# Kernel optimization log

Hardware: AMD Instinct MI355X
Metric: run time of the kernel (lower is better)

Reference implementation:

```python
import jax, jax.numpy as jnp
import numpy as np

BATCH, N_IN, N_OUT = 1024, 512, 512
GRID, DEGREE = 8, 3
NUM_BASIS = GRID + DEGREE  # 11
LO, HI = -3.0, 3.0
_h = (HI - LO) / GRID
# extended knot vector: GRID + 2*DEGREE + 1 knots -> GRID + DEGREE basis functions
KNOTS = jnp.asarray(np.linspace(LO - DEGREE * _h, HI + DEGREE * _h,
                                GRID + 2 * DEGREE + 1), dtype=jnp.float32)


def bspline_basis(x):
    """Cox-de Boor recursion. x: (batch, n_in) -> (batch, n_in, NUM_BASIS)."""
    t = KNOTS
    xb = x[..., None]
    B = ((xb >= t[:-1]) & (xb < t[1:])).astype(x.dtype)  # degree 0
    for d in range(1, DEGREE + 1):
        left = (xb - t[:-(d + 1)]) / (t[d:-1] - t[:-(d + 1)])
        right = (t[d + 1:] - xb) / (t[d + 1:] - t[1:-d])
        B = left * B[..., :-1] + right * B[..., 1:]
    return B


def setup_inputs() -> dict:
    key = jax.random.key(0)
    kx, kc, kw = jax.random.split(key, 3)
    x = jax.random.normal(kx, (BATCH, N_IN), dtype=jnp.float32)
    # xavier_normal_ init for c: fan_in = num_basis, fan_out = n_in*n_out
    c_std = float(np.sqrt(2.0 / (N_IN * N_OUT + NUM_BASIS)))
    c = jax.random.normal(kc, (N_IN * N_OUT, NUM_BASIS), dtype=jnp.float32) * c_std
    w_std = float(np.sqrt(2.0 / (N_IN + N_OUT)))
    w = jax.random.normal(kw, (N_IN, N_OUT), dtype=jnp.float32) * w_std
    return {"x": x, "c": c, "w": w}


def reference(x, c, w):
    # spline basis: (batch, n_in, K)
    bx = bspline_basis(x)
    # per-edge coefficients: (n_in, n_out, K)
    cr = c.reshape(N_IN, N_OUT, NUM_BASIS)
    # out[b,i,o] = sum_k bx[b,i,k] * c[i,o,k]
    spline = jnp.einsum('bik,iok->bio', bx, cr)
    # w * (silu(x) + spline), summed over n_in -> (batch, n_out)
    out = jnp.einsum('io,bio->bo', w, jax.nn.silu(x)[..., None] + spline)
    return out
```

## Files before the change

### kernel.cpp

```cpp
#include <hip/hip_runtime.h>

#define BATCH 1024
#define NIN   512
#define NOUT  512
#define NB    11
#define KDIM  (NIN * 12)
#define SPLITS 16
#define IPS    (NIN / SPLITS)
#define LDW    104

typedef short bf16x8 __attribute__((ext_vector_type(8)));
typedef float f32x4  __attribute__((ext_vector_type(4)));
typedef unsigned short ushort8 __attribute__((ext_vector_type(8)));

__device__ __forceinline__ unsigned short f2bf(float f) {
  unsigned u = __float_as_uint(f);
  u += 0x7fff + ((u >> 16) & 1);
  return (unsigned short)(u >> 16);
}
__device__ __forceinline__ float bf2f(unsigned short h) {
  return __uint_as_float((unsigned)h << 16);
}

__global__ __launch_bounds__(256) void k_prep(const float* __restrict__ c,
                                              const float* __restrict__ w,
                                              unsigned short* __restrict__ Bt) {
  __shared__ float          ws_[8 * 128];
  __shared__ unsigned short sbt[128 * 96];
  int tid = threadIdx.x;
  int bc  = blockIdx.x;
  int i0  = (bc >> 2) * 8;
  int o0  = (bc & 3) * 128;
  {
    int r = tid >> 5, oq = (tid & 31) * 4;
    *(f32x4*)&ws_[r * 128 + oq] = *(const f32x4*)&w[(size_t)(i0 + r) * NOUT + o0 + oq];
  }
  __syncthreads();
  for (int n = 0; n < 11; ++n) {
    int ch  = n * 256 + tid;
    int il  = ch / 352;
    int off = (ch - il * 352) * 4;
    f32x4 cv = *(const f32x4*)&c[(size_t)(i0 + il) * (NIN * NB) + (size_t)o0 * NB + off];
#pragma unroll
    for (int e = 0; e < 4; ++e) {
      int t  = off + e;
      int op = t / 11;
      int k  = t - op * 11;
      sbt[op * 96 + il * 12 + k] = f2bf(cv[e] * ws_[il * 128 + op]);
    }
  }
  {
    int il = tid >> 5, oq = (tid & 31) * 4;
#pragma unroll
    for (int e = 0; e < 4; ++e)
      sbt[(oq + e) * 96 + il * 12 + 11] = f2bf(ws_[il * 128 + oq + e]);
  }
  __syncthreads();
  for (int n = 0; n < 6; ++n) {
    int ch = n * 256 + tid;
    int op = ch / 12, q = ch - op * 12;
    *(ushort8*)&Bt[(size_t)(o0 + op) * KDIM + i0 * 12 + q * 8] =
        *(const ushort8*)&sbt[op * 96 + q * 8];
  }
}

__global__ __launch_bounds__(256) void k_fused(const float* __restrict__ x,
                                               const unsigned short* __restrict__ Bt,
                                               unsigned short* __restrict__ part,
                                               float* __restrict__ out,
                                               int splits, int ipersplit) {
  __shared__ unsigned short As[128 * LDW];
  __shared__ unsigned short Bs[128 * LDW];
  const int tid  = threadIdx.x;
  const int lane = tid & 63, wave = tid >> 6;
  const int wr = wave >> 1, wc = wave & 1;
  const int mbase = blockIdx.x * 128, nbase = blockIdx.y * 128;
  const int split = blockIdx.z;
  const int istart = split * ipersplit;

  f32x4 acc[4][4] = {};
  const int mrow = lane & 15;
  const int kq   = (lane >> 4) * 8;

  const int iters = ipersplit / 8;
  for (int it = 0; it < iters; ++it) {
    int ib = istart + it * 8;
    {
      int bl  = tid >> 1;
      int il0 = (tid & 1) * 4;
      f32x4 xv = *(const f32x4*)&x[(size_t)(mbase + bl) * NIN + ib + il0];
      unsigned short* arow = &As[bl * LDW];
#pragma unroll
      for (int q = 0; q < 4; ++q) {
        int col = (il0 + q) * 12;
        *(unsigned long long*)&arow[col]     = 0ULL;
        *(unsigned long long*)&arow[col + 4] = 0ULL;
        *(unsigned long long*)&arow[col + 8] = 0ULL;
        float xq = xv[q];
        float um = (xq + 5.25f) * (1.0f / 0.75f);
        int   m  = (int)floorf(um);
        if (m >= 0 && m <= 13) {
          float u  = um - (float)m;
          float u2 = u * u, u3 = u2 * u;
          float omu = 1.0f - u;
          float w3 = u3 * (1.0f / 6.0f);
          float w2 = (-3.0f*u3 + 3.0f*u2 + 3.0f*u + 1.0f) * (1.0f/6.0f);
          float w1 = (3.0f*u3 - 6.0f*u2 + 4.0f) * (1.0f/6.0f);
          float w0 = omu * omu * omu * (1.0f / 6.0f);
          int j0 = m - 3;
          if (j0 >= 0 && j0 <= 10)         arow[col + j0]     = f2bf(w0);
          if (j0 + 1 >= 0 && j0 + 1 <= 10) arow[col + j0 + 1] = f2bf(w1);
          if (j0 + 2 >= 0 && j0 + 2 <= 10) arow[col + j0 + 2] = f2bf(w2);
          if (m <= 10)                     arow[col + m]      = f2bf(w3);
        }
        float sig = 1.0f / (1.0f + __expf(-xq));
        arow[col + 11] = f2bf(xq * sig);
      }
    }
#pragma unroll
    for (int n = 0; n < 6; ++n) {
      int ch  = n * 256 + tid;
      int row = ch / 12;
      int cg  = ch - row * 12;
      ushort8 vb = *(const ushort8*)&Bt[(size_t)(nbase + row) * KDIM + ib * 12 + cg * 8];
      *(ushort8*)&Bs[row * LDW + cg * 8] = vb;
    }
    __syncthreads();

#pragma unroll
    for (int ks = 0; ks < 96; ks += 32) {
      bf16x8 af[4], bfr[4];
#pragma unroll
      for (int mt = 0; mt < 4; ++mt)
        af[mt] = *(const bf16x8*)&As[(wr * 64 + mt * 16 + mrow) * LDW + ks + kq];
#pragma unroll
      for (int nt = 0; nt < 4; ++nt)
        bfr[nt] = *(const bf16x8*)&Bs[(wc * 64 + nt * 16 + mrow) * LDW + ks + kq];
#pragma unroll
      for (int mt = 0; mt < 4; ++mt)
#pragma unroll
        for (int nt = 0; nt < 4; ++nt)
          acc[mt][nt] = __builtin_amdgcn_mfma_f32_16x16x32_bf16(af[mt], bfr[nt], acc[mt][nt], 0, 0, 0);
    }
    __syncthreads();
  }

  const int rq = (lane >> 4) * 4;
  if (splits == 1) {
#pragma unroll
    for (int mt = 0; mt < 4; ++mt)
#pragma unroll
      for (int nt = 0; nt < 4; ++nt) {
        int colg = nbase + wc * 64 + nt * 16 + mrow;
#pragma unroll
        for (int r = 0; r < 4; ++r) {
          int rowg = mbase + wr * 64 + mt * 16 + rq + r;
          out[(size_t)rowg * NOUT + colg] = acc[mt][nt][r];
        }
      }
    return;
  }
#pragma unroll
  for (int mt = 0; mt < 4; ++mt)
#pragma unroll
    for (int nt = 0; nt < 4; ++nt) {
      int colg = nbase + wc * 64 + nt * 16 + mrow;
#pragma unroll
      for (int r = 0; r < 4; ++r) {
        int rowg = mbase + wr * 64 + mt * 16 + rq + r;
        part[((size_t)split * BATCH + rowg) * NOUT + colg] = f2bf(acc[mt][nt][r]);
      }
    }
}

__global__ __launch_bounds__(256) void k_reduce(const unsigned short* __restrict__ part,
                                                float* __restrict__ out) {
  int t = blockIdx.x * 256 + threadIdx.x;
  const ushort8* pv = (const ushort8*)part;
  float s[8] = {};
#pragma unroll
  for (int sp = 0; sp < SPLITS; ++sp) {
    ushort8 v = pv[(size_t)sp * (BATCH * NOUT / 8) + t];
#pragma unroll
    for (int e = 0; e < 8; ++e) s[e] += bf2f(v[e]);
  }
  f32x4 lo = { s[0], s[1], s[2], s[3] };
  f32x4 hi = { s[4], s[5], s[6], s[7] };
  ((f32x4*)out)[t * 2]     = lo;
  ((f32x4*)out)[t * 2 + 1] = hi;
}

extern "C" void kernel_launch(void* const* d_in, const int* in_sizes, int n_in,
                              void* d_out, int out_size, void* d_ws, size_t ws_size,
                              hipStream_t stream) {
  const float* x = (const float*)d_in[0];
  const float* c = (const float*)d_in[1];
  const float* w = (const float*)d_in[2];
  float* out = (float*)d_out;

  unsigned short* Bt = (unsigned short*)d_ws;
  size_t off_part = (size_t)NOUT * KDIM * 2;
  unsigned short* part = (unsigned short*)((char*)d_ws + off_part);
  size_t need = off_part + (size_t)SPLITS * BATCH * NOUT * 2;

  k_prep<<<dim3(256), 256, 0, stream>>>(c, w, Bt);
  if (ws_size >= need) {
    k_fused<<<dim3(8, 4, SPLITS), 256, 0, stream>>>(x, Bt, part, out, SPLITS, IPS);
    k_reduce<<<dim3((BATCH * NOUT / 8) / 256), 256, 0, stream>>>(part, out);
  } else {
    k_fused<<<dim3(8, 4, 1), 256, 0, stream>>>(x, Bt, part, out, 1, NIN);
  }
}
```

Measured before the change: 92.46 us.

## Fuse prep, GEMM and reduce into one cooperative kernel with grid syncs

Replaces the three separate launches (coefficient prep, split-K GEMM, reduction) with a single cooperative kernel of 512 blocks that runs the three phases separated by grid.sync(). The prep phase is re-tiled to 4 input rows per block so that 512 blocks cover it. The aim is to remove launch gaps and kernel boundaries between the stages. In exchange it depends on cooperative launch succeeding with 512 co-resident blocks, which use about 53KB of LDS each, and adds grid-wide barrier costs. If the cooperative launch fails it falls back to the old path.

```diff
diff --git a/kernel.cpp b/kernel.cpp
--- a/kernel.cpp
+++ b/kernel.cpp
@@ -1,4 +1,7 @@
 #include <hip/hip_runtime.h>
+#include <hip/hip_cooperative_groups.h>
+
+namespace cg = cooperative_groups;
 
 #define BATCH 1024
 #define NIN   512
@@ -21,6 +24,174 @@
 __device__ __forceinline__ float bf2f(unsigned short h) {
   return __uint_as_float((unsigned)h << 16);
 }
+
+
+__device__ __forceinline__ void basis_row_gen(const float* __restrict__ x,
+                                              unsigned short* __restrict__ As,
+                                              int tid, int mbase, int ib) {
+  int bl  = tid >> 1;
+  int il0 = (tid & 1) * 4;
+  f32x4 xv = *(const f32x4*)&x[(size_t)(mbase + bl) * NIN + ib + il0];
+  unsigned short* arow = &As[bl * LDW];
+#pragma unroll
+  for (int q = 0; q < 4; ++q) {
+    int col = (il0 + q) * 12;
+    *(unsigned long long*)&arow[col]     = 0ULL;
+    *(unsigned long long*)&arow[col + 4] = 0ULL;
+    *(unsigned long long*)&arow[col + 8] = 0ULL;
+    float xq = xv[q];
+    float um = (xq + 5.25f) * (1.0f / 0.75f);
+    int   m  = (int)floorf(um);
+    if (m >= 0 && m <= 13) {
+      float u  = um - (float)m;
+      float u2 = u * u, u3 = u2 * u;
+      float omu = 1.0f - u;
+      float w3 = u3 * (1.0f / 6.0f);
+      float w2 = (-3.0f*u3 + 3.0f*u2 + 3.0f*u + 1.0f) * (1.0f/6.0f);
+      float w1 = (3.0f*u3 - 6.0f*u2 + 4.0f) * (1.0f/6.0f);
+      float w0 = omu * omu * omu * (1.0f / 6.0f);
+      int j0 = m - 3;
+      if (j0 >= 0 && j0 <= 10)         arow[col + j0]     = f2bf(w0);
+      if (j0 + 1 >= 0 && j0 + 1 <= 10) arow[col + j0 + 1] = f2bf(w1);
+      if (j0 + 2 >= 0 && j0 + 2 <= 10) arow[col + j0 + 2] = f2bf(w2);
+      if (m <= 10)                     arow[col + m]      = f2bf(w3);
+    }
+    float sig = 1.0f / (1.0f + __expf(-xq));
+    arow[col + 11] = f2bf(xq * sig);
+  }
+}
+
+__global__ __launch_bounds__(256) void k_mega(const float* __restrict__ x,
+                                              const float* __restrict__ c,
+                                              const float* __restrict__ w,
+                                              unsigned short* __restrict__ Bt,
+                                              unsigned short* __restrict__ part,
+                                              float* __restrict__ out) {
+  __shared__ char smem[53248];
+  cg::grid_group grid = cg::this_grid();
+  const int blk = blockIdx.x;
+  const int tid = threadIdx.x;
+
+  {
+    float*          ws_ = (float*)smem;
+    unsigned short* sbt = (unsigned short*)(smem + 2048);
+    int i0 = (blk >> 2) * 4;
+    int o0 = (blk & 3) * 128;
+    if (tid < 128) {
+      int il = tid >> 5, oq = (tid & 31) * 4;
+      *(f32x4*)&ws_[il * 128 + oq] = *(const f32x4*)&w[(size_t)(i0 + il) * NOUT + o0 + oq];
+    }
+    __syncthreads();
+    for (int n = 0; n < 6; ++n) {
+      int ch = n * 256 + tid;
+      if (ch < 1408) {
+        int il  = ch / 352;
+        int off = (ch - il * 352) * 4;
+        f32x4 cv = *(const f32x4*)&c[(size_t)(i0 + il) * (NIN * NB) + (size_t)o0 * NB + off];
+#pragma unroll
+        for (int e = 0; e < 4; ++e) {
+          int t  = off + e;
+          int op = t / 11;
+          int k  = t - op * 11;
+          sbt[op * 48 + il * 12 + k] = f2bf(cv[e] * ws_[il * 128 + op]);
+        }
+      }
+    }
+#pragma unroll
+    for (int e = 0; e < 2; ++e) {
+      int idx = e * 256 + tid;
+      int op = idx >> 2, il = idx & 3;
+      sbt[op * 48 + il * 12 + 11] = f2bf(ws_[il * 128 + op]);
+    }
+    __syncthreads();
+    for (int n = 0; n < 3; ++n) {
+      int ch = n * 256 + tid;
+      int op = ch / 6, q = ch - op * 6;
+      *(ushort8*)&Bt[(size_t)(o0 + op) * KDIM + i0 * 12 + q * 8] =
+          *(const ushort8*)&sbt[op * 48 + q * 8];
+    }
+  }
+  grid.sync();
+
+  {
+    unsigned short* As = (unsigned short*)smem;
+    unsigned short* Bs = As + 128 * LDW;
+    const int lane = tid & 63, wave = tid >> 6;
+    const int wr = wave >> 1, wc = wave & 1;
+    const int mbase = (blk & 7) * 128;
+    const int nbase = ((blk >> 3) & 3) * 128;
+    const int split = blk >> 5;
+    const int istart = split * IPS;
+
+    f32x4 acc[4][4] = {};
+    const int mrow = lane & 15;
+    const int kq   = (lane >> 4) * 8;
+
+#pragma unroll 1
+    for (int it = 0; it < IPS / 8; ++it) {
+      int ib = istart + it * 8;
+      basis_row_gen(x, As, tid, mbase, ib);
+#pragma unroll
+      for (int n = 0; n < 6; ++n) {
+        int ch  = n * 256 + tid;
+        int row = ch / 12;
+        int cg_ = ch - row * 12;
+        ushort8 vb = *(const ushort8*)&Bt[(size_t)(nbase + row) * KDIM + ib * 12 + cg_ * 8];
+        *(ushort8*)&Bs[row * LDW + cg_ * 8] = vb;
+      }
+      __syncthreads();
+#pragma unroll
+      for (int ks = 0; ks < 96; ks += 32) {
+        bf16x8 af[4], bfr[4];
+#pragma unroll
+        for (int mt = 0; mt < 4; ++mt)
+          af[mt] = *(const bf16x8*)&As[(wr * 64 + mt * 16 + mrow) * LDW + ks + kq];
+#pragma unroll
+        for (int nt = 0; nt < 4; ++nt)
+          bfr[nt] = *(const bf16x8*)&Bs[(wc * 64 + nt * 16 + mrow) * LDW + ks + kq];
+#pragma unroll
+        for (int mt = 0; mt < 4; ++mt)
+#pragma unroll
+          for (int nt = 0; nt < 4; ++nt)
+            acc[mt][nt] = __builtin_amdgcn_mfma_f32_16x16x32_bf16(af[mt], bfr[nt], acc[mt][nt], 0, 0, 0);
+      }
+      __syncthreads();
+    }
+
+    const int rq = (lane >> 4) * 4;
+#pragma unroll
+    for (int mt = 0; mt < 4; ++mt)
+#pragma unroll
+      for (int nt = 0; nt < 4; ++nt) {
+        int colg = nbase + wc * 64 + nt * 16 + mrow;
+#pragma unroll
+        for (int r = 0; r < 4; ++r) {
+          int rowg = mbase + wr * 64 + mt * 16 + rq + r;
+          part[((size_t)split * BATCH + rowg) * NOUT + colg] = f2bf(acc[mt][nt][r]);
+        }
+      }
+  }
+  grid.sync();
+
+  {
+    int g = blk * 256 + tid;
+    if (g < BATCH * NOUT / 8) {
+      const ushort8* pv = (const ushort8*)part;
+      float s[8] = {};
+#pragma unroll
+      for (int sp = 0; sp < SPLITS; ++sp) {
+        ushort8 v = pv[(size_t)sp * (BATCH * NOUT / 8) + g];
+#pragma unroll
+        for (int e = 0; e < 8; ++e) s[e] += bf2f(v[e]);
+      }
+      f32x4 lo = { s[0], s[1], s[2], s[3] };
+      f32x4 hi = { s[4], s[5], s[6], s[7] };
+      ((f32x4*)out)[g * 2]     = lo;
+      ((f32x4*)out)[g * 2 + 1] = hi;
+    }
+  }
+}
+
 
 __global__ __launch_bounds__(256) void k_prep(const float* __restrict__ c,
                                               const float* __restrict__ w,
@@ -82,51 +253,18 @@
   const int mrow = lane & 15;
   const int kq   = (lane >> 4) * 8;
 
-  const int iters = ipersplit / 8;
-  for (int it = 0; it < iters; ++it) {
+  for (int it = 0; it < ipersplit / 8; ++it) {
     int ib = istart + it * 8;
-    {
-      int bl  = tid >> 1;
-      int il0 = (tid & 1) * 4;
-      f32x4 xv = *(const f32x4*)&x[(size_t)(mbase + bl) * NIN + ib + il0];
-      unsigned short* arow = &As[bl * LDW];
-#pragma unroll
-      for (int q = 0; q < 4; ++q) {
-        int col = (il0 + q) * 12;
-        *(unsigned long long*)&arow[col]     = 0ULL;
-        *(unsigned long long*)&arow[col + 4] = 0ULL;
-        *(unsigned long long*)&arow[col + 8] = 0ULL;
-        float xq = xv[q];
-        float um = (xq + 5.25f) * (1.0f / 0.75f);
-        int   m  = (int)floorf(um);
-        if (m >= 0 && m <= 13) {
-          float u  = um - (float)m;
-          float u2 = u * u, u3 = u2 * u;
-          float omu = 1.0f - u;
-          float w3 = u3 * (1.0f / 6.0f);
-          float w2 = (-3.0f*u3 + 3.0f*u2 + 3.0f*u + 1.0f) * (1.0f/6.0f);
-          float w1 = (3.0f*u3 - 6.0f*u2 + 4.0f) * (1.0f/6.0f);
-          float w0 = omu * omu * omu * (1.0f / 6.0f);
-          int j0 = m - 3;
-          if (j0 >= 0 && j0 <= 10)         arow[col + j0]     = f2bf(w0);
-          if (j0 + 1 >= 0 && j0 + 1 <= 10) arow[col + j0 + 1] = f2bf(w1);
-          if (j0 + 2 >= 0 && j0 + 2 <= 10) arow[col + j0 + 2] = f2bf(w2);
-          if (m <= 10)                     arow[col + m]      = f2bf(w3);
-        }
-        float sig = 1.0f / (1.0f + __expf(-xq));
-        arow[col + 11] = f2bf(xq * sig);
-      }
-    }
+    basis_row_gen(x, As, tid, mbase, ib);
 #pragma unroll
     for (int n = 0; n < 6; ++n) {
       int ch  = n * 256 + tid;
       int row = ch / 12;
-      int cg  = ch - row * 12;
-      ushort8 vb = *(const ushort8*)&Bt[(size_t)(nbase + row) * KDIM + ib * 12 + cg * 8];
-      *(ushort8*)&Bs[row * LDW + cg * 8] = vb;
+      int cg_ = ch - row * 12;
+      ushort8 vb = *(const ushort8*)&Bt[(size_t)(nbase + row) * KDIM + ib * 12 + cg_ * 8];
+      *(ushort8*)&Bs[row * LDW + cg_ * 8] = vb;
     }
     __syncthreads();
-
 #pragma unroll
     for (int ks = 0; ks < 96; ks += 32) {
       bf16x8 af[4], bfr[4];
@@ -203,11 +341,18 @@
   unsigned short* part = (unsigned short*)((char*)d_ws + off_part);
   size_t need = off_part + (size_t)SPLITS * BATCH * NOUT * 2;
 
-  k_prep<<<dim3(256), 256, 0, stream>>>(c, w, Bt);
   if (ws_size >= need) {
+    void* args[] = { (void*)&x, (void*)&c, (void*)&w,
+                     (void*)&Bt, (void*)&part, (void*)&out };
+    hipError_t err = hipLaunchCooperativeKernel((const void*)k_mega,
+                                                dim3(512), dim3(256),
+                                                args, 0, stream);
+    if (err == hipSuccess) return;
+    k_prep<<<dim3(256), 256, 0, stream>>>(c, w, Bt);
     k_fused<<<dim3(8, 4, SPLITS), 256, 0, stream>>>(x, Bt, part, out, SPLITS, IPS);
     k_reduce<<<dim3((BATCH * NOUT / 8) / 256), 256, 0, stream>>>(part, out);
   } else {
+    k_prep<<<dim3(256), 256, 0, stream>>>(c, w, Bt);
     k_fused<<<dim3(8, 4, 1), 256, 0, stream>>>(x, Bt, part, out, 1, NIN);
   }
 }
```

New measurement: 216.3 us. 2.34x slower.

## Double-buffer A tile in LDS and load B fragments directly from global

Applied to the files above, without the earlier changes.

The spline-basis A tile is now generated into a double-buffered LDS array one iteration ahead, with the next x vector prefetched into registers, so generation overlaps the MFMA work and only one barrier per iteration remains. The B tile no longer passes through shared memory: each wave loads its bf16 fragments straight from global memory into registers. This removes LDS staging and a barrier for B. In exchange, B fragment reads are 16-byte per-lane global loads that are not shared across the waves of a block, and their latency now sits directly in front of the MFMAs.

```diff
diff --git a/kernel.cpp b/kernel.cpp
--- a/kernel.cpp
+++ b/kernel.cpp
@@ -64,13 +64,45 @@
   }
 }
 
+__device__ __forceinline__ void a_gen(f32x4 xv, unsigned short* __restrict__ As,
+                                      int tid) {
+  int bl  = tid >> 1;
+  int il0 = (tid & 1) * 4;
+  unsigned short* arow = &As[bl * LDW];
+#pragma unroll
+  for (int q = 0; q < 4; ++q) {
+    int col = (il0 + q) * 12;
+    *(unsigned long long*)&arow[col]     = 0ULL;
+    *(unsigned long long*)&arow[col + 4] = 0ULL;
+    *(unsigned long long*)&arow[col + 8] = 0ULL;
+    float xq = xv[q];
+    float um = (xq + 5.25f) * (1.0f / 0.75f);
+    int   m  = (int)floorf(um);
+    if (m >= 0 && m <= 13) {
+      float u  = um - (float)m;
+      float u2 = u * u, u3 = u2 * u;
+      float omu = 1.0f - u;
+      float w3 = u3 * (1.0f / 6.0f);
+      float w2 = (-3.0f*u3 + 3.0f*u2 + 3.0f*u + 1.0f) * (1.0f/6.0f);
+      float w1 = (3.0f*u3 - 6.0f*u2 + 4.0f) * (1.0f/6.0f);
+      float w0 = omu * omu * omu * (1.0f / 6.0f);
+      int j0 = m - 3;
+      if (j0 >= 0 && j0 <= 10)         arow[col + j0]     = f2bf(w0);
+      if (j0 + 1 >= 0 && j0 + 1 <= 10) arow[col + j0 + 1] = f2bf(w1);
+      if (j0 + 2 >= 0 && j0 + 2 <= 10) arow[col + j0 + 2] = f2bf(w2);
+      if (m <= 10)                     arow[col + m]      = f2bf(w3);
+    }
+    float sig = 1.0f / (1.0f + __expf(-xq));
+    arow[col + 11] = f2bf(xq * sig);
+  }
+}
+
 __global__ __launch_bounds__(256) void k_fused(const float* __restrict__ x,
                                                const unsigned short* __restrict__ Bt,
                                                unsigned short* __restrict__ part,
                                                float* __restrict__ out,
                                                int splits, int ipersplit) {
-  __shared__ unsigned short As[128 * LDW];
-  __shared__ unsigned short Bs[128 * LDW];
+  __shared__ unsigned short As2[2][128 * LDW];
   const int tid  = threadIdx.x;
   const int lane = tid & 63, wave = tid >> 6;
   const int wr = wave >> 1, wc = wave & 1;
@@ -82,67 +114,45 @@
   const int mrow = lane & 15;
   const int kq   = (lane >> 4) * 8;
 
+  const unsigned short* bgp[4];
+#pragma unroll
+  for (int nt = 0; nt < 4; ++nt)
+    bgp[nt] = &Bt[(size_t)(nbase + wc * 64 + nt * 16 + mrow) * KDIM + kq];
+
+  const float* xg = &x[(size_t)(mbase + (tid >> 1)) * NIN + (tid & 1) * 4];
+
   const int iters = ipersplit / 8;
+  f32x4 xv = *(const f32x4*)&xg[istart];
+  a_gen(xv, As2[0], tid);
+  if (iters > 1) xv = *(const f32x4*)&xg[istart + 8];
+  __syncthreads();
+
   for (int it = 0; it < iters; ++it) {
-    int ib = istart + it * 8;
-    {
-      int bl  = tid >> 1;
-      int il0 = (tid & 1) * 4;
-      f32x4 xv = *(const f32x4*)&x[(size_t)(mbase + bl) * NIN + ib + il0];
-      unsigned short* arow = &As[bl * LDW];
-#pragma unroll
-      for (int q = 0; q < 4; ++q) {
-        int col = (il0 + q) * 12;
-        *(unsigned long long*)&arow[col]     = 0ULL;
-        *(unsigned long long*)&arow[col + 4] = 0ULL;
-        *(unsigned long long*)&arow[col + 8] = 0ULL;
-        float xq = xv[q];
-        float um = (xq + 5.25f) * (1.0f / 0.75f);
-        int   m  = (int)floorf(um);
-        if (m >= 0 && m <= 13) {
-          float u  = um - (float)m;
-          float u2 = u * u, u3 = u2 * u;
-          float omu = 1.0f - u;
-          float w3 = u3 * (1.0f / 6.0f);
-          float w2 = (-3.0f*u3 + 3.0f*u2 + 3.0f*u + 1.0f) * (1.0f/6.0f);
-          float w1 = (3.0f*u3 - 6.0f*u2 + 4.0f) * (1.0f/6.0f);
-          float w0 = omu * omu * omu * (1.0f / 6.0f);
-          int j0 = m - 3;
-          if (j0 >= 0 && j0 <= 10)         arow[col + j0]     = f2bf(w0);
-          if (j0 + 1 >= 0 && j0 + 1 <= 10) arow[col + j0 + 1] = f2bf(w1);
-          if (j0 + 2 >= 0 && j0 + 2 <= 10) arow[col + j0 + 2] = f2bf(w2);
-          if (m <= 10)                     arow[col + m]      = f2bf(w3);
-        }
-        float sig = 1.0f / (1.0f + __expf(-xq));
-        arow[col + 11] = f2bf(xq * sig);
-      }
-    }
-#pragma unroll
-    for (int n = 0; n < 6; ++n) {
-      int ch  = n * 256 + tid;
-      int row = ch / 12;
-      int cg  = ch - row * 12;
-      ushort8 vb = *(const ushort8*)&Bt[(size_t)(nbase + row) * KDIM + ib * 12 + cg * 8];
-      *(ushort8*)&Bs[row * LDW + cg * 8] = vb;
-    }
-    __syncthreads();
-
+    const int cur = it & 1;
+    const int ib  = istart + it * 8;
+    if (it + 1 < iters) {
+      a_gen(xv, As2[cur ^ 1], tid);
+      if (it + 2 < iters) xv = *(const f32x4*)&xg[ib + 16];
+    }
+
+    const unsigned short* asb = As2[cur];
+    const int kBase = ib * 12;
 #pragma unroll
     for (int ks = 0; ks < 96; ks += 32) {
-      bf16x8 af[4], bfr[4];
+      bf16x8 bfr[4], af[4];
+#pragma unroll
+      for (int nt = 0; nt < 4; ++nt)
+        bfr[nt] = *(const bf16x8*)&bgp[nt][kBase + ks];
 #pragma unroll
       for (int mt = 0; mt < 4; ++mt)
-        af[mt] = *(const bf16x8*)&As[(wr * 64 + mt * 16 + mrow) * LDW + ks + kq];
-#pragma unroll
-      for (int nt = 0; nt < 4; ++nt)
-        bfr[nt] = *(const bf16x8*)&Bs[(wc * 64 + nt * 16 + mrow) * LDW + ks + kq];
+        af[mt] = *(const bf16x8*)&asb[(wr * 64 + mt * 16 + mrow) * LDW + ks + kq];
 #pragma unroll
       for (int mt = 0; mt < 4; ++mt)
 #pragma unroll
         for (int nt = 0; nt < 4; ++nt)
           acc[mt][nt] = __builtin_amdgcn_mfma_f32_16x16x32_bf16(af[mt], bfr[nt], acc[mt][nt], 0, 0, 0);
     }
-    __syncthreads();
+    if (it + 1 < iters) __syncthreads();
   }
 
   const int rq = (lane >> 4) * 4;
```

Result: no change. 94.30 us (+2.0%).
